# Kernel optimization log

Measured on AMD Instinct MI355X. Metric: run time of the kernel, lower is better.

The kernel has to match this reference:

```python
import jax, jax.numpy as jnp
import numpy as np

WS = 7        # window_size
SHIFT = 3     # shift_size
HEADS = 12
EMBED = 384


def _relative_position_index(ws: int) -> np.ndarray:
    coords = np.stack(np.meshgrid(np.arange(ws), np.arange(ws), indexing='ij'))  # [2,ws,ws]
    flat = coords.reshape(2, -1)                                                 # [2,ws*ws]
    rel = flat[:, :, None] - flat[:, None, :]                                     # [2,N,N]
    rel = rel.transpose(1, 2, 0)
    rel[:, :, 0] += ws - 1
    rel[:, :, 1] += ws - 1
    rel[:, :, 0] *= 2 * ws - 1
    return rel.sum(-1)  # [ws*ws, ws*ws]


def setup_inputs() -> dict:
    key = jax.random.key(0)
    ks = jax.random.split(key, 6)
    B, H, W, C = 32, 56, 56, EMBED
    x = jax.random.normal(ks[0], (B, H * W, C), dtype=jnp.float32)
    s = 0.02
    qkv_w = jax.random.normal(ks[1], (C, 3 * C), dtype=jnp.float32) * s
    qkv_b = jnp.zeros((3 * C,), dtype=jnp.float32)
    proj_w = jax.random.normal(ks[2], (C, C), dtype=jnp.float32) * s
    proj_b = jnp.zeros((C,), dtype=jnp.float32)
    rel_bias_table = jax.random.normal(ks[3], ((2 * WS - 1) ** 2, HEADS), dtype=jnp.float32) * s
    return {"x": x, "qkv_w": qkv_w, "qkv_b": qkv_b, "proj_w": proj_w,
            "proj_b": proj_b, "rel_bias_table": rel_bias_table, "H": H, "W": W}


def reference(x, qkv_w, qkv_b, proj_w, proj_b, rel_bias_table, H, W):
    B, L, C = x.shape
    hd = C // HEADS
    scale = hd ** (-0.5)
    ws = WS
    x = x.reshape(B, H, W, C)
    # pad to multiples of window size (static python ints)
    pad_r = (ws - W % ws) % ws
    pad_b_ = (ws - H % ws) % ws
    if pad_r or pad_b_:
        x = jnp.pad(x, ((0, 0), (0, pad_b_), (0, pad_r), (0, 0)))
    Hp, Wp = H + pad_b_, W + pad_r
    # cyclic shift
    if SHIFT > 0:
        x = jnp.roll(x, shift=(-SHIFT, -SHIFT), axis=(1, 2))
    # window partition -> [nW, ws*ws, C]
    nh, nw = Hp // ws, Wp // ws
    xw = x.reshape(B, nh, ws, nw, ws, C).transpose(0, 1, 3, 2, 4, 5).reshape(-1, ws * ws, C)
    # qkv projection
    qkv = xw @ qkv_w + qkv_b                               # [nW, N, 3C]
    qkv = qkv.reshape(-1, ws * ws, 3, HEADS, hd).transpose(2, 0, 3, 1, 4)
    q, k, v = qkv[0], qkv[1], qkv[2]                        # [nW, heads, N, hd]
    attn = jnp.einsum('whnd,whmd->whnm', q, k) * scale
    rpi = jnp.asarray(_relative_position_index(ws))         # [N, N] static
    bias = rel_bias_table[rpi.reshape(-1)].reshape(ws * ws, ws * ws, HEADS)
    attn = attn + bias.transpose(2, 0, 1)[None]             # [1, heads, N, N]
    attn = jax.nn.softmax(attn, axis=-1)
    out = jnp.einsum('whnm,whmd->whnd', attn, v)            # [nW, heads, N, hd]
    out = out.transpose(0, 2, 1, 3).reshape(-1, ws, ws, C)
    # merge windows
    out = out.reshape(B, nh, nw, ws, ws, C).transpose(0, 1, 3, 2, 4, 5).reshape(B, Hp, Wp, C)
    if SHIFT > 0:
        out = jnp.roll(out, shift=(SHIFT, SHIFT), axis=(1, 2))
    if pad_r or pad_b_:
        out = out[:, :H, :W, :]
    out = out.reshape(B, H * W, C)
    return out @ proj_w + proj_b
```

## Files before the change

kernel.cpp:

```cpp
#include <hip/hip_runtime.h>


typedef __attribute__((ext_vector_type(8))) short short8;
typedef __attribute__((ext_vector_type(4))) float floatx4;

#define CDIM  384
#define QKVN  1152
#define MROWS 100352
#define LROW  3136

static constexpr size_t QKV_ELEMS = 38535168ull;
static constexpr size_t OFF_Q    = 0;
static constexpr size_t OFF_K    = OFF_Q  + QKV_ELEMS * 2 + 4096;
static constexpr size_t OFF_V    = OFF_K  + QKV_ELEMS * 2 + 4096;
static constexpr size_t OFF_AO   = OFF_V  + QKV_ELEMS * 2 + 4096;
static constexpr size_t OFF_WQ   = OFF_AO + (size_t)MROWS * CDIM * 2 + 4096;
static constexpr size_t OFF_WP   = OFF_WQ + (size_t)QKVN * CDIM * 2 + 256;
static constexpr size_t OFF_BIAS = OFF_WP + (size_t)CDIM * CDIM * 2 + 256;
static constexpr size_t OFF_LUT  = OFF_BIAS + (size_t)12 * 64 * 64 * 4 + 256;

__device__ __forceinline__ unsigned short f2bf(float f) {
  unsigned int u = __float_as_uint(f);
  unsigned int lsb = (u >> 16) & 1u;
  u += 0x7fffu + lsb;
  return (unsigned short)(u >> 16);
}

__device__ __forceinline__ void gl2lds16(const void* g, void* l) {
  __builtin_amdgcn_global_load_lds(
      (const __attribute__((address_space(1))) unsigned int*)g,
      (__attribute__((address_space(3))) unsigned int*)l, 16, 0, 0);
}

#define RAW_BARRIER()                           \
  do {                                          \
    __builtin_amdgcn_sched_barrier(0);          \
    asm volatile("s_barrier" ::: "memory");     \
    __builtin_amdgcn_sched_barrier(0);          \
  } while (0)
#define WAIT_VM(N)                                        \
  do {                                                    \
    asm volatile("s_waitcnt vmcnt(" #N ")" ::: "memory"); \
    __builtin_amdgcn_sched_barrier(0);                    \
  } while (0)

__global__ __launch_bounds__(256) void prep_kernel(
    const float* __restrict__ x, const float* __restrict__ qkv_w,
    const float* __restrict__ proj_w, const float* __restrict__ rbt,
    char* __restrict__ ws) {
  unsigned short* Wq = (unsigned short*)(ws + OFF_WQ);
  unsigned short* Wp = (unsigned short*)(ws + OFF_WP);
  unsigned short* XB = (unsigned short*)(ws + OFF_AO);
  float* biasp = (float*)(ws + OFF_BIAS);
  int* lut = (int*)(ws + OFF_LUT);
  const int tid = blockIdx.x * blockDim.x + threadIdx.x;
  const int stride = gridDim.x * blockDim.x;
  for (int idx = tid; idx < QKVN * CDIM; idx += stride) {
    int n = idx / CDIM, k = idx - n * CDIM;
    Wq[idx] = f2bf(qkv_w[(size_t)k * QKVN + n]);
  }
  for (int idx = tid; idx < CDIM * CDIM; idx += stride) {
    int n = idx / CDIM, k = idx - n * CDIM;
    Wp[idx] = f2bf(proj_w[(size_t)k * CDIM + n]);
  }
  for (int idx = tid; idx < 12 * 64 * 64; idx += stride) {
    int h = idx / 4096;
    int rem = idx - h * 4096;
    int lane = rem / 64;
    int e = rem - lane * 64;
    int fm = e >> 4, fn = (e >> 2) & 3, r = e & 3;
    int row = fm * 16 + (lane >> 4) * 4 + r;
    int col = fn * 16 + (lane & 15);
    float v = -1e30f;
    if (row < 49 && col < 49) {
      int i = row / 7, j = row - i * 7;
      int k2 = col / 7, l2 = col - k2 * 7;
      int rpi = (i - k2 + 6) * 13 + (j - l2 + 6);
      v = rbt[rpi * 12 + h];
    }
    biasp[idx] = v;
  }
  for (int idx = tid; idx < MROWS; idx += stride) {
    int b_ = idx / LROW, l = idx - b_ * LROW;
    int y = l / 56, xx = l - y * 56;
    int yr = y + 53; if (yr >= 56) yr -= 56;
    int xr = xx + 53; if (xr >= 56) xr -= 56;
    int win = b_ * 64 + (yr / 7) * 8 + (xr / 7);
    int nidx = (yr % 7) * 7 + (xr % 7);
    lut[idx] = win * 18816 + nidx * 32;
  }
  const size_t n8 = (size_t)MROWS * CDIM / 8;
  for (size_t idx = tid; idx < n8; idx += stride) {
    const float4* s = (const float4*)(x + idx * 8);
    float4 f0 = s[0], f1 = s[1];
    uint4 o;
    o.x = (unsigned)f2bf(f0.x) | ((unsigned)f2bf(f0.y) << 16);
    o.y = (unsigned)f2bf(f0.z) | ((unsigned)f2bf(f0.w) << 16);
    o.z = (unsigned)f2bf(f1.x) | ((unsigned)f2bf(f1.y) << 16);
    o.w = (unsigned)f2bf(f1.z) | ((unsigned)f2bf(f1.w) << 16);
    ((uint4*)XB)[idx] = o;
  }
}

__global__ __launch_bounds__(256) void qkv_gemm(
    const float* __restrict__ qkv_b, char* __restrict__ ws) {
  __shared__ unsigned short As[2][128][32];
  __shared__ unsigned short Bs[2][128][32];
  const unsigned short* XB = (const unsigned short*)(ws + OFF_AO);
  const unsigned short* Wq = (const unsigned short*)(ws + OFF_WQ);
  unsigned short* Qb = (unsigned short*)(ws + OFF_Q);
  unsigned short* Kb = (unsigned short*)(ws + OFF_K);
  unsigned short* Vb = (unsigned short*)(ws + OFF_V);
  const int* lut = (const int*)(ws + OFF_LUT);
  const int L = blockIdx.x;
  const int xcd = L & 7, slot = L >> 3;
  const int g9 = slot / 9;
  const int m0 = (g9 * 8 + xcd) * 128;
  const int n0 = (slot - g9 * 9) * 128;
  const int t = threadIdx.x;
  const int lane = t & 63, li = lane & 15, qd = lane >> 4;
  const int wv = t >> 6, wm = wv >> 1, wn = wv & 1;
  const int ld_r = lane >> 2;
  const int ld_c = (lane & 3) * 8;
  const unsigned short* agp = XB + (size_t)(m0 + wv * 32 + ld_r) * CDIM + ld_c;
  const unsigned short* bgp = Wq + (size_t)(n0 + wv * 32 + ld_r) * CDIM + ld_c;

#define QSTAGE(buf, k0)                                          \
  do {                                                           \
    gl2lds16(agp + (k0),             &As[buf][wv * 32][0]);      \
    gl2lds16(agp + (k0) + 16 * CDIM, &As[buf][wv * 32 + 16][0]); \
    gl2lds16(bgp + (k0),             &Bs[buf][wv * 32][0]);      \
    gl2lds16(bgp + (k0) + 16 * CDIM, &Bs[buf][wv * 32 + 16][0]); \
  } while (0)

  floatx4 acc[4][4] = {};
  QSTAGE(0, 0);
  QSTAGE(1, 32);
  for (int kt = 0; kt < 12; ++kt) {
    const int cur = kt & 1;
    if (kt < 11) { WAIT_VM(4); }
    else         { WAIT_VM(0); }
    RAW_BARRIER();
    short8 a[4], b[4];
#pragma unroll
    for (int f = 0; f < 4; f++)
      a[f] = *(const short8*)&As[cur][wm * 64 + f * 16 + li][qd * 8];
#pragma unroll
    for (int f = 0; f < 4; f++)
      b[f] = *(const short8*)&Bs[cur][wn * 64 + f * 16 + li][qd * 8];
#pragma unroll
    for (int i = 0; i < 4; i++)
#pragma unroll
      for (int j = 0; j < 4; j++)
        acc[i][j] = __builtin_amdgcn_mfma_f32_16x16x32_bf16(a[i], b[j], acc[i][j], 0, 0, 0);
    RAW_BARRIER();
    if (kt + 2 < 12) QSTAGE(cur, (kt + 2) * 32);
  }
#undef QSTAGE

  const int which = n0 / CDIM;
  unsigned short* dst = which == 0 ? Qb : (which == 1 ? Kb : Vb);
  const float mul = (which == 0) ? 0.17677669529663689f : 1.0f;
#pragma unroll
  for (int i = 0; i < 4; i++) {
    int lbase[4];
#pragma unroll
    for (int r = 0; r < 4; r++)
      lbase[r] = lut[m0 + wm * 64 + i * 16 + qd * 4 + r];
#pragma unroll
    for (int j = 0; j < 4; j++) {
      int c = n0 + wn * 64 + j * 16 + li;
      int cc = c - which * CDIM;
      int head = cc >> 5, d = cc & 31;
      int hd_off = head * 1568 + d;
      float bval = qkv_b[c];
#pragma unroll
      for (int r = 0; r < 4; r++) {
        size_t off = (size_t)(lbase[r] + hd_off);
        dst[off] = f2bf((acc[i][j][r] + bval) * mul);
      }
    }
  }
}

__global__ __launch_bounds__(256) void attn_kernel(char* __restrict__ ws) {
  __shared__ unsigned short SMEM[4][64 * 72];
  const int win = blockIdx.x;
  const int t = threadIdx.x, wv = t >> 6, lane = t & 63;
  const int h = blockIdx.y * 4 + wv;
  const int li = lane & 15, qd = lane >> 4;
  unsigned short* Sm = &SMEM[wv][0];
  const size_t whoff = (size_t)(win * 12 + h) * 49 * 32;
  const unsigned short* Qb = (const unsigned short*)(ws + OFF_Q) + whoff;
  const unsigned short* Kb = (const unsigned short*)(ws + OFF_K) + whoff;
  const unsigned short* Vb = (const unsigned short*)(ws + OFF_V) + whoff;
  const float* biasp = (const float*)(ws + OFF_BIAS) + ((size_t)h * 64 + lane) * 64;

  short8 qa[4], kb4[4];
#pragma unroll
  for (int f = 0; f < 4; f++) {
    qa[f] = *(const short8*)(Qb + (f * 16 + li) * 32 + qd * 8);
    kb4[f] = *(const short8*)(Kb + (f * 16 + li) * 32 + qd * 8);
  }

  for (int idx = lane; idx < 512; idx += 64) {
    Sm[(idx >> 4) * 72 + 48 + (idx & 15)] = 0;
  }
  {
    const uint2* vsrc = (const uint2*)Vb;
    for (int idx = lane; idx < 392; idx += 64) {
      uint2 dv = vsrc[idx];
      int row = idx >> 3, d0 = (idx & 7) * 4;
      Sm[(d0 + 0) * 72 + row] = (unsigned short)(dv.x & 0xffff);
      Sm[(d0 + 1) * 72 + row] = (unsigned short)(dv.x >> 16);
      Sm[(d0 + 2) * 72 + row] = (unsigned short)(dv.y & 0xffff);
      Sm[(d0 + 3) * 72 + row] = (unsigned short)(dv.y >> 16);
    }
  }

  floatx4 s[4][4] = {};
#pragma unroll
  for (int i = 0; i < 4; i++)
#pragma unroll
    for (int j = 0; j < 4; j++)
      s[i][j] = __builtin_amdgcn_mfma_f32_16x16x32_bf16(qa[i], kb4[j], s[i][j], 0, 0, 0);

  short8 vb[2][2];
#pragma unroll
  for (int ss = 0; ss < 2; ss++)
#pragma unroll
    for (int nf = 0; nf < 2; nf++)
      vb[ss][nf] = *(const short8*)&Sm[(nf * 16 + li) * 72 + ss * 32 + qd * 8];

  float rsum[4][4];
#pragma unroll
  for (int fm = 0; fm < 4; fm++) {
#pragma unroll
    for (int fn = 0; fn < 4; fn++) {
      floatx4 bv = *(const floatx4*)(biasp + (fm * 4 + fn) * 4);
#pragma unroll
      for (int r = 0; r < 4; r++)
        s[fm][fn][r] = __expf(s[fm][fn][r] + bv[r]);
    }
#pragma unroll
    for (int r = 0; r < 4; r++) {
      float v = s[fm][0][r] + s[fm][1][r] + s[fm][2][r] + s[fm][3][r];
      v += __shfl_xor(v, 1);
      v += __shfl_xor(v, 2);
      v += __shfl_xor(v, 4);
      v += __shfl_xor(v, 8);
      rsum[fm][r] = v;
    }
#pragma unroll
    for (int fn = 0; fn < 4; fn++)
#pragma unroll
      for (int r = 0; r < 4; r++)
        Sm[(fm * 16 + qd * 4 + r) * 72 + fn * 16 + li] = f2bf(s[fm][fn][r]);
  }

  floatx4 o[4][2] = {};
#pragma unroll
  for (int fm = 0; fm < 4; fm++)
#pragma unroll
    for (int ss = 0; ss < 2; ss++) {
      short8 pa = *(const short8*)&Sm[(fm * 16 + li) * 72 + ss * 32 + qd * 8];
#pragma unroll
      for (int nf = 0; nf < 2; nf++)
        o[fm][nf] = __builtin_amdgcn_mfma_f32_16x16x32_bf16(pa, vb[ss][nf], o[fm][nf], 0, 0, 0);
    }

  unsigned short* AO = (unsigned short*)(ws + OFF_AO);
  const int b_ = win >> 6, wrem = win & 63, wy = wrem >> 3, wx = wrem & 7;
#pragma unroll
  for (int fm = 0; fm < 4; fm++)
#pragma unroll
    for (int r = 0; r < 4; r++) {
      int n = fm * 16 + qd * 4 + r;
      if (n >= 49) continue;
      float inv = 1.0f / rsum[fm][r];
      int i_ = n / 7, j_ = n - i_ * 7;
      int y = wy * 7 + i_ + 3;  if (y >= 56) y -= 56;
      int xx = wx * 7 + j_ + 3; if (xx >= 56) xx -= 56;
      size_t base = ((size_t)b_ * LROW + y * 56 + xx) * CDIM + h * 32;
#pragma unroll
      for (int nf = 0; nf < 2; nf++)
        AO[base + nf * 16 + li] = f2bf(o[fm][nf][r] * inv);
    }
}

__global__ __launch_bounds__(256) void proj_gemm(
    const float* __restrict__ proj_b, char* __restrict__ ws,
    float* __restrict__ out) {
  __shared__ unsigned short As[2][128][32];
  __shared__ unsigned short Bs[2][128][32];
  const unsigned short* AO = (const unsigned short*)(ws + OFF_AO);
  const unsigned short* Wp = (const unsigned short*)(ws + OFF_WP);
  const int L = blockIdx.x;
  const int xcd = L & 7, slot = L >> 3;
  const int g3 = slot / 3;
  const int m0 = (g3 * 8 + xcd) * 128;
  const int n0 = (slot - g3 * 3) * 128;
  const int t = threadIdx.x;
  const int lane = t & 63, li = lane & 15, qd = lane >> 4;
  const int wv = t >> 6, wm = wv >> 1, wn = wv & 1;
  const int ld_r = lane >> 2;
  const int ld_c = (lane & 3) * 8;
  const unsigned short* agp = AO + (size_t)(m0 + wv * 32 + ld_r) * CDIM + ld_c;
  const unsigned short* bgp = Wp + (size_t)(n0 + wv * 32 + ld_r) * CDIM + ld_c;

#define PSTAGE(buf, k0)                                          \
  do {                                                           \
    gl2lds16(agp + (k0),             &As[buf][wv * 32][0]);      \
    gl2lds16(agp + (k0) + 16 * CDIM, &As[buf][wv * 32 + 16][0]); \
    gl2lds16(bgp + (k0),             &Bs[buf][wv * 32][0]);      \
    gl2lds16(bgp + (k0) + 16 * CDIM, &Bs[buf][wv * 32 + 16][0]); \
  } while (0)

  floatx4 acc[4][4] = {};
  PSTAGE(0, 0);
  PSTAGE(1, 32);
  for (int kt = 0; kt < 12; ++kt) {
    const int cur = kt & 1;
    if (kt < 11) { WAIT_VM(4); }
    else         { WAIT_VM(0); }
    RAW_BARRIER();
    short8 a[4], b[4];
#pragma unroll
    for (int f = 0; f < 4; f++)
      a[f] = *(const short8*)&As[cur][wm * 64 + f * 16 + li][qd * 8];
#pragma unroll
    for (int f = 0; f < 4; f++)
      b[f] = *(const short8*)&Bs[cur][wn * 64 + f * 16 + li][qd * 8];
#pragma unroll
    for (int i = 0; i < 4; i++)
#pragma unroll
      for (int j = 0; j < 4; j++)
        acc[i][j] = __builtin_amdgcn_mfma_f32_16x16x32_bf16(a[i], b[j], acc[i][j], 0, 0, 0);
    RAW_BARRIER();
    if (kt + 2 < 12) PSTAGE(cur, (kt + 2) * 32);
  }
#undef PSTAGE

#pragma unroll
  for (int i = 0; i < 4; i++)
#pragma unroll
    for (int j = 0; j < 4; j++) {
      int c = n0 + wn * 64 + j * 16 + li;
      float bv = proj_b[c];
#pragma unroll
      for (int r = 0; r < 4; r++) {
        int m = m0 + wm * 64 + i * 16 + qd * 4 + r;
        out[(size_t)m * CDIM + c] = acc[i][j][r] + bv;
      }
    }
}

extern "C" void kernel_launch(void* const* d_in, const int* in_sizes, int n_in,
                              void* d_out, int out_size, void* d_ws, size_t ws_size,
                              hipStream_t stream) {
  const float* x      = (const float*)d_in[0];
  const float* qkv_w  = (const float*)d_in[1];
  const float* qkv_b  = (const float*)d_in[2];
  const float* proj_w = (const float*)d_in[3];
  const float* proj_b = (const float*)d_in[4];
  const float* rbt    = (const float*)d_in[5];
  char* ws = (char*)d_ws;
  float* out = (float*)d_out;

  prep_kernel<<<2048, 256, 0, stream>>>(x, qkv_w, proj_w, rbt, ws);
  qkv_gemm<<<7056, 256, 0, stream>>>(qkv_b, ws);
  attn_kernel<<<dim3(2048, 3), 256, 0, stream>>>(ws);
  proj_gemm<<<2352, 256, 0, stream>>>(proj_b, ws, out);
}
```

Baseline: 613.4 us.

## Load GEMM MFMA operands directly from global memory, dropping LDS staging

Both the QKV and projection GEMMs stop staging A/B tiles through double-buffered LDS with global_load_lds and barriers. Each wave now loads its MFMA fragments straight from global memory into registers inside a fully unrolled K loop. This removes LDS traffic, barriers and waitcnt synchronisation. In exchange, operand loads shared between waves are duplicated and rely on L1/L2 caching, and register pressure rises from the unrolled loads.

```diff
diff --git a/kernel.cpp b/kernel.cpp
--- a/kernel.cpp
+++ b/kernel.cpp
@@ -25,24 +25,6 @@
   u += 0x7fffu + lsb;
   return (unsigned short)(u >> 16);
 }
-
-__device__ __forceinline__ void gl2lds16(const void* g, void* l) {
-  __builtin_amdgcn_global_load_lds(
-      (const __attribute__((address_space(1))) unsigned int*)g,
-      (__attribute__((address_space(3))) unsigned int*)l, 16, 0, 0);
-}
-
-#define RAW_BARRIER()                           \
-  do {                                          \
-    __builtin_amdgcn_sched_barrier(0);          \
-    asm volatile("s_barrier" ::: "memory");     \
-    __builtin_amdgcn_sched_barrier(0);          \
-  } while (0)
-#define WAIT_VM(N)                                        \
-  do {                                                    \
-    asm volatile("s_waitcnt vmcnt(" #N ")" ::: "memory"); \
-    __builtin_amdgcn_sched_barrier(0);                    \
-  } while (0)
 
 __global__ __launch_bounds__(256) void prep_kernel(
     const float* __restrict__ x, const float* __restrict__ qkv_w,
@@ -104,8 +86,6 @@
 
 __global__ __launch_bounds__(256) void qkv_gemm(
     const float* __restrict__ qkv_b, char* __restrict__ ws) {
-  __shared__ unsigned short As[2][128][32];
-  __shared__ unsigned short Bs[2][128][32];
   const unsigned short* XB = (const unsigned short*)(ws + OFF_AO);
   const unsigned short* Wq = (const unsigned short*)(ws + OFF_WQ);
   unsigned short* Qb = (unsigned short*)(ws + OFF_Q);
@@ -120,43 +100,29 @@
   const int t = threadIdx.x;
   const int lane = t & 63, li = lane & 15, qd = lane >> 4;
   const int wv = t >> 6, wm = wv >> 1, wn = wv & 1;
-  const int ld_r = lane >> 2;
-  const int ld_c = (lane & 3) * 8;
-  const unsigned short* agp = XB + (size_t)(m0 + wv * 32 + ld_r) * CDIM + ld_c;
-  const unsigned short* bgp = Wq + (size_t)(n0 + wv * 32 + ld_r) * CDIM + ld_c;
-
-#define QSTAGE(buf, k0)                                          \
-  do {                                                           \
-    gl2lds16(agp + (k0),             &As[buf][wv * 32][0]);      \
-    gl2lds16(agp + (k0) + 16 * CDIM, &As[buf][wv * 32 + 16][0]); \
-    gl2lds16(bgp + (k0),             &Bs[buf][wv * 32][0]);      \
-    gl2lds16(bgp + (k0) + 16 * CDIM, &Bs[buf][wv * 32 + 16][0]); \
-  } while (0)
+
+  const unsigned short* ap[4];
+  const unsigned short* bp[4];
+#pragma unroll
+  for (int f = 0; f < 4; f++) {
+    ap[f] = XB + (size_t)(m0 + wm * 64 + f * 16 + li) * CDIM + qd * 8;
+    bp[f] = Wq + (size_t)(n0 + wn * 64 + f * 16 + li) * CDIM + qd * 8;
+  }
 
   floatx4 acc[4][4] = {};
-  QSTAGE(0, 0);
-  QSTAGE(1, 32);
+#pragma unroll
   for (int kt = 0; kt < 12; ++kt) {
-    const int cur = kt & 1;
-    if (kt < 11) { WAIT_VM(4); }
-    else         { WAIT_VM(0); }
-    RAW_BARRIER();
     short8 a[4], b[4];
 #pragma unroll
-    for (int f = 0; f < 4; f++)
-      a[f] = *(const short8*)&As[cur][wm * 64 + f * 16 + li][qd * 8];
-#pragma unroll
-    for (int f = 0; f < 4; f++)
-      b[f] = *(const short8*)&Bs[cur][wn * 64 + f * 16 + li][qd * 8];
+    for (int f = 0; f < 4; f++) a[f] = *(const short8*)(ap[f] + kt * 32);
+#pragma unroll
+    for (int f = 0; f < 4; f++) b[f] = *(const short8*)(bp[f] + kt * 32);
 #pragma unroll
     for (int i = 0; i < 4; i++)
 #pragma unroll
       for (int j = 0; j < 4; j++)
         acc[i][j] = __builtin_amdgcn_mfma_f32_16x16x32_bf16(a[i], b[j], acc[i][j], 0, 0, 0);
-    RAW_BARRIER();
-    if (kt + 2 < 12) QSTAGE(cur, (kt + 2) * 32);
-  }
-#undef QSTAGE
+  }
 
   const int which = n0 / CDIM;
   unsigned short* dst = which == 0 ? Qb : (which == 1 ? Kb : Vb);
@@ -291,8 +257,6 @@
 __global__ __launch_bounds__(256) void proj_gemm(
     const float* __restrict__ proj_b, char* __restrict__ ws,
     float* __restrict__ out) {
-  __shared__ unsigned short As[2][128][32];
-  __shared__ unsigned short Bs[2][128][32];
   const unsigned short* AO = (const unsigned short*)(ws + OFF_AO);
   const unsigned short* Wp = (const unsigned short*)(ws + OFF_WP);
   const int L = blockIdx.x;
@@ -303,43 +267,29 @@
   const int t = threadIdx.x;
   const int lane = t & 63, li = lane & 15, qd = lane >> 4;
   const int wv = t >> 6, wm = wv >> 1, wn = wv & 1;
-  const int ld_r = lane >> 2;
-  const int ld_c = (lane & 3) * 8;
-  const unsigned short* agp = AO + (size_t)(m0 + wv * 32 + ld_r) * CDIM + ld_c;
-  const unsigned short* bgp = Wp + (size_t)(n0 + wv * 32 + ld_r) * CDIM + ld_c;
-
-#define PSTAGE(buf, k0)                                          \
-  do {                                                           \
-    gl2lds16(agp + (k0),             &As[buf][wv * 32][0]);      \
-    gl2lds16(agp + (k0) + 16 * CDIM, &As[buf][wv * 32 + 16][0]); \
-    gl2lds16(bgp + (k0),             &Bs[buf][wv * 32][0]);      \
-    gl2lds16(bgp + (k0) + 16 * CDIM, &Bs[buf][wv * 32 + 16][0]); \
-  } while (0)
+
+  const unsigned short* ap[4];
+  const unsigned short* bp[4];
+#pragma unroll
+  for (int f = 0; f < 4; f++) {
+    ap[f] = AO + (size_t)(m0 + wm * 64 + f * 16 + li) * CDIM + qd * 8;
+    bp[f] = Wp + (size_t)(n0 + wn * 64 + f * 16 + li) * CDIM + qd * 8;
+  }
 
   floatx4 acc[4][4] = {};
-  PSTAGE(0, 0);
-  PSTAGE(1, 32);
+#pragma unroll
   for (int kt = 0; kt < 12; ++kt) {
-    const int cur = kt & 1;
-    if (kt < 11) { WAIT_VM(4); }
-    else         { WAIT_VM(0); }
-    RAW_BARRIER();
     short8 a[4], b[4];
 #pragma unroll
-    for (int f = 0; f < 4; f++)
-      a[f] = *(const short8*)&As[cur][wm * 64 + f * 16 + li][qd * 8];
-#pragma unroll
-    for (int f = 0; f < 4; f++)
-      b[f] = *(const short8*)&Bs[cur][wn * 64 + f * 16 + li][qd * 8];
+    for (int f = 0; f < 4; f++) a[f] = *(const short8*)(ap[f] + kt * 32);
+#pragma unroll
+    for (int f = 0; f < 4; f++) b[f] = *(const short8*)(bp[f] + kt * 32);
 #pragma unroll
     for (int i = 0; i < 4; i++)
 #pragma unroll
       for (int j = 0; j < 4; j++)
         acc[i][j] = __builtin_amdgcn_mfma_f32_16x16x32_bf16(a[i], b[j], acc[i][j], 0, 0, 0);
-    RAW_BARRIER();
-    if (kt + 2 < 12) PSTAGE(cur, (kt + 2) * 32);
-  }
-#undef PSTAGE
+  }
 
 #pragma unroll
   for (int i = 0; i < 4; i++)
```

After: 841.5 us. +37.2%, slower.
